# Kernel tuning notes

Measured on AMD Instinct MI355X. Metric: run time of the kernel, lower is better.

The kernel has to match this reference:

```python
import jax, jax.numpy as jnp
import numpy as np

EPS = 1e-12
B, T, D, N, FF, NH = 8, 512, 768, 6, 3072, 12
DH = D // NH  # attention head size = 64


def lin(x, w, b):
    # torch nn.Linear: y = x @ W^T + b, W: [out, in]
    return x @ w.T + b


def layer_norm(x, w, b):
    m = x.mean(-1, keepdims=True)
    v = ((x - m) ** 2).mean(-1, keepdims=True)
    return (x - m) / jnp.sqrt(v + EPS) * w + b


def conv1d(x, w, b, pad):
    # x: [B,T,D] -> conv over T with D channels -> [B,T,D]; w: [out,in,k]
    y = jax.lax.conv_general_dilated(jnp.transpose(x, (0, 2, 1)), w, (1,), [(pad, pad)],
                                     dimension_numbers=('NCH', 'OIH', 'NCH'))
    return jnp.transpose(y + b[None, :, None], (0, 2, 1))


def gelu(x):
    return jax.nn.gelu(x, approximate=False)


def setup_inputs() -> dict:
    key = jax.random.key(0)
    ks = iter(jax.random.split(key, 64))
    std = 0.02
    nrm = lambda shape: jax.random.normal(next(ks), shape, jnp.float32) * std
    inp = {}
    for i in range(N):
        inp[f'f{i}'] = jax.random.normal(next(ks), (B, T, D), jnp.float32)
    inp['Ea'] = jax.random.normal(next(ks), (B, T, D), jnp.float32)
    inp['align_w'] = nrm((N, D, D)); inp['align_b'] = jnp.zeros((N, D))
    # MultiFeatureFusion attention_fc: Linear(12, 6)
    inp['att_w'] = nrm((N, 2 * N)); inp['att_b'] = jnp.zeros((N,))
    # GatedFusion
    inp['g1_w'] = nrm((2 * D, 2 * D)); inp['g1_b'] = jnp.zeros((2 * D,))
    inp['g2_w'] = nrm((2 * D, 2 * D)); inp['g2_b'] = jnp.zeros((2 * D,))
    inp['g3_w'] = nrm((D, 2 * D)); inp['g3_b'] = jnp.zeros((D,))
    inp['g4_w'] = nrm((D, D)); inp['g4_b'] = jnp.zeros((D,))
    # MSFastformer shared LayerNorm + multi-scale convs
    inp['ln_w'] = jnp.ones((D,)); inp['ln_b'] = jnp.zeros((D,))
    inp['c1_w'] = nrm((D, D, 1)); inp['c1_b'] = jnp.zeros((D,))
    inp['c3_w'] = nrm((D, D, 3)); inp['c3_b'] = jnp.zeros((D,))
    inp['c5_w'] = nrm((D, D, 5)); inp['c5_b'] = jnp.zeros((D,))
    # FastformerLayer (shared across the three P branches)
    inp['q_w'] = nrm((D, D)); inp['q_b'] = jnp.zeros((D,))
    inp['qa_w'] = nrm((NH, D)); inp['qa_b'] = jnp.zeros((NH,))
    inp['k_w'] = nrm((D, D)); inp['k_b'] = jnp.zeros((D,))
    inp['ka_w'] = nrm((NH, D)); inp['ka_b'] = jnp.zeros((NH,))
    inp['tr_w'] = nrm((D, D)); inp['tr_b'] = jnp.zeros((D,))
    inp['ao_w'] = nrm((D, D)); inp['ao_b'] = jnp.zeros((D,))
    inp['fln_w'] = jnp.ones((D,)); inp['fln_b'] = jnp.zeros((D,))
    inp['fi_w'] = nrm((FF, D)); inp['fi_b'] = jnp.zeros((FF,))
    inp['fo_w'] = nrm((D, FF)); inp['fo_b'] = jnp.zeros((D,))
    # MSFastformer FFN + output projection
    inp['m1_w'] = nrm((FF, D)); inp['m1_b'] = jnp.zeros((FF,))
    inp['m2_w'] = nrm((D, FF)); inp['m2_b'] = jnp.zeros((D,))
    inp['out_w'] = nrm((D, D)); inp['out_b'] = jnp.zeros((D,))
    return inp


def reference(f0, f1, f2, f3, f4, f5, Ea,
              align_w, align_b, att_w, att_b,
              g1_w, g1_b, g2_w, g2_b, g3_w, g3_b, g4_w, g4_b,
              ln_w, ln_b, c1_w, c1_b, c3_w, c3_b, c5_w, c5_b,
              q_w, q_b, qa_w, qa_b, k_w, k_b, ka_w, ka_b, tr_w, tr_b, ao_w, ao_b,
              fln_w, fln_b, fi_w, fi_b, fo_w, fo_b,
              m1_w, m1_b, m2_w, m2_b, out_w, out_b):
    scale = 1.0 / (DH ** 0.5)

    def fastformer_layer(hid, ctx):
        # FastSelfAttention (note: scores contract over heads -> [B,S,Sc])
        q = lin(hid, q_w, q_b)                      # [B,S,D]
        kk = lin(ctx, k_w, k_b)                     # [B,Sc,D]
        qs = lin(q, qa_w, qa_b) * scale             # [B,S,H]
        ks = lin(kk, ka_w, ka_b) * scale            # [B,Sc,H]
        scores = jnp.einsum('bsh,bch->bsc', qs, ks)
        aw = jax.nn.softmax(scores, axis=-1)
        ctx_layer = jnp.einsum('bsc,bcd->bsd', aw, kk)
        self_out = lin(ctx_layer, tr_w, tr_b) + q
        # FastAttention residual + FFN sublayer
        att = lin(self_out, ao_w, ao_b) + hid
        att = layer_norm(att, fln_w, fln_b)
        inter = gelu(lin(att, fi_w, fi_b))
        out = lin(inter, fo_w, fo_b) + att
        return layer_norm(out, fln_w, fln_b)

    # --- FeatureAlignment: 1x1 convs (all lengths equal -> no interpolation) ---
    F6 = jnp.stack([f0, f1, f2, f3, f4, f5])                         # [N,B,T,D]
    A = jnp.einsum('nbtd,ned->nbte', F6, align_w) + align_b[:, None, None, :]
    H = jnp.transpose(A, (1, 0, 3, 2))                               # [B,N,D,T]

    # --- MultiFeatureFusion: mean_T.mean(D) and mean_D.mean(T) both equal full mean ---
    m = H.mean(axis=(2, 3))                                          # [B,N]
    mean_features = jnp.concatenate([m, m], axis=1)                  # [B,2N]
    w = jax.nn.softmax(jax.nn.relu(lin(mean_features, att_w, att_b)), axis=1)
    fused = (H * w[:, :, None, None]).sum(axis=1) + H.mean(axis=1)   # [B,D,T]
    Et = jnp.transpose(fused, (0, 2, 1))                             # [B,T,D]

    # --- GatedFusion (dropout = identity, eval mode) ---
    cc = jnp.concatenate([Et, Ea], axis=-1)
    o = jax.nn.relu(lin(cc, g1_w, g1_b))
    o = jax.nn.relu(lin(o, g2_w, g2_b))
    o = jax.nn.relu(lin(o, g3_w, g3_b))
    g = jax.nn.sigmoid(lin(o, g4_w, g4_b))
    Ef = g * Ea + (1.0 - g) * Et

    # --- MSFastformer ---
    x = layer_norm(Ef, ln_w, ln_b)
    U1 = conv1d(x, c1_w, c1_b, 0)
    U3 = conv1d(x, c3_w, c3_b, 1)
    U5 = conv1d(x, c5_w, c5_b, 2)
    P = fastformer_layer(U5, U3) + fastformer_layer(U3, U1) + fastformer_layer(U1, U5)
    Pn = layer_norm(P, ln_w, ln_b)
    I = lin(gelu(lin(Pn, m1_w, m1_b)), m2_w, m2_b)
    J = I + x
    y = lin(layer_norm(J, ln_w, ln_b), out_w, out_b)
    return y
```

## Files before the change

kernel.cpp:

```cpp
#include <hip/hip_runtime.h>
#include <math.h>


typedef unsigned short u16;
typedef __attribute__((ext_vector_type(8))) short short8;
typedef __attribute__((ext_vector_type(8))) unsigned short us8;
typedef __attribute__((ext_vector_type(4))) float floatx4;
typedef unsigned __attribute__((address_space(1))) gu32;
typedef unsigned __attribute__((address_space(3))) lu32;

#define DD 768
#define TT 512
#define BB 8
#define MM 4096
#define FFN 3072
#define MDL ((long)MM * DD)

__device__ __forceinline__ float b2f(u16 u) {
  union { unsigned u32; float f; } x; x.u32 = ((unsigned)u) << 16; return x.f;
}
__device__ __forceinline__ u16 f2b(float f) {
  union { float f; unsigned u; } x; x.f = f;
  unsigned r = x.u + 0x7FFFu + ((x.u >> 16) & 1u);
  return (u16)(r >> 16);
}

template<int BM, int BN, int OP>
__global__ __launch_bounds__(256)
void gemm_bt(const u16* __restrict__ A, const u16* __restrict__ W,
             const float* __restrict__ bias, const float* __restrict__ rowBias,
             const void* __restrict__ residv, void* __restrict__ Cv,
             int N, int K, int ldc, int rBf16, int outBf16,
             int ntaps, int pad, long wtapStride,
             long aBatch, long wBatch, long cBatch, long rBatch,
             const u16* __restrict__ zp)
{
  __shared__ __align__(16) u16 sA[2][BM * 64];
  __shared__ __align__(16) u16 sB[2][BN * 64];
  const int tid  = threadIdx.x;
  const int lane = tid & 63;
  const int wv   = tid >> 6;

  int gx = gridDim.x, gy = gridDim.y;
  int bn = blockIdx.y * gx + blockIdx.x;
  int Tt = gx * gy;
  if ((Tt & 7) == 0) bn = (bn & 7) * (Tt >> 3) + (bn >> 3);
  const int m0 = (bn / gx) * BM;
  const int n0 = (bn % gx) * BN;
  const u16* Ab  = A + (long)blockIdx.z * aBatch;
  const u16* Wb0 = W + (long)blockIdx.z * wBatch;

  constexpr int NI = (BM == 128 && BN == 128) ? 4 : (BM == 128 ? 2 : 1);
  constexpr int NJ = 4;
  int wr, wc;
  if constexpr (BM == 128 && BN == 128) { wr = (wv >> 1) * 64; wc = (wv & 1) * 64; }
  else if constexpr (BM == 128)          { wr = wv * 32;        wc = 0; }
  else                                    { wr = wv * 16;        wc = 0; }

  floatx4 acc[NI][NJ];
#pragma unroll
  for (int i = 0; i < NI; ++i)
#pragma unroll
    for (int j = 0; j < NJ; ++j) acc[i][j] = (floatx4){0.f, 0.f, 0.f, 0.f};

  const int mrow = lane & 15;
  const int ksub = (lane >> 4) * 8;

  auto STAGE = [&](int tap_, int k0_, int bsel) {
    const int dt = tap_ - pad;
    const u16* Wt = Wb0 + (long)tap_ * wtapStride;
    u16* sAb = &sA[bsel][0];
    u16* sBb = &sB[bsel][0];
#pragma unroll
    for (int it = 0; it < BM / 32; ++it) {
      int slot = it * 256 + tid;
      int row = slot >> 3;
      int col = ((slot ^ row) & 7) * 8;
      int gr = m0 + row;
      int t  = gr & (TT - 1);
      const u16* src = ((unsigned)(t + dt) < (unsigned)TT)
                     ? (Ab + (long)(gr + dt) * K + k0_ + col) : zp;
      __builtin_amdgcn_global_load_lds((const gu32*)src,
                                       (lu32*)((char*)sAb + slot * 16), 16, 0, 0);
    }
#pragma unroll
    for (int it = 0; it < BN / 32; ++it) {
      int slot = it * 256 + tid;
      int row = slot >> 3;
      int col = ((slot ^ row) & 7) * 8;
      const u16* src = Wt + (long)(n0 + row) * K + k0_ + col;
      __builtin_amdgcn_global_load_lds((const gu32*)src,
                                       (lu32*)((char*)sBb + slot * 16), 16, 0, 0);
    }
  };

  const int nk = K >> 6;
  const int nsteps = ntaps * nk;

  STAGE(0, 0, 0);
  asm volatile("s_waitcnt vmcnt(0)" ::: "memory");
  __builtin_amdgcn_s_barrier();

  int tap = 0, k0 = 0, cur = 0;
  for (int s = 0; s < nsteps; ++s) {
    int ntap = tap, nk0 = k0 + 64;
    if (nk0 >= K) { nk0 = 0; ntap = tap + 1; }
    if (s + 1 < nsteps) STAGE(ntap, nk0, cur ^ 1);
    {
      const u16* sAb = &sA[cur][0];
      const u16* sBb = &sB[cur][0];
#pragma unroll
      for (int kb = 0; kb < 64; kb += 32) {
        const int ch0 = (kb + ksub) >> 3;
        short8 af[NI], bfr[NJ];
#pragma unroll
        for (int i = 0; i < NI; ++i) {
          int ra = wr + i * 16 + mrow;
          af[i] = *(const short8*)(sAb + ra * 64 + ((ch0 ^ (ra & 7)) << 3));
        }
#pragma unroll
        for (int j = 0; j < NJ; ++j) {
          int rb = wc + j * 16 + mrow;
          bfr[j] = *(const short8*)(sBb + rb * 64 + ((ch0 ^ (rb & 7)) << 3));
        }
#pragma unroll
        for (int i = 0; i < NI; ++i)
#pragma unroll
          for (int j = 0; j < NJ; ++j)
            acc[i][j] = __builtin_amdgcn_mfma_f32_16x16x32_bf16(af[i], bfr[j], acc[i][j], 0, 0, 0);
      }
    }
    asm volatile("s_waitcnt vmcnt(0)" ::: "memory");
    __builtin_amdgcn_s_barrier();
    cur ^= 1; tap = ntap; k0 = nk0;
  }

  const int cn = lane & 15;
  const int rq = (lane >> 4) * 4;
  u16*   Ch = (u16*)Cv   + (long)blockIdx.z * cBatch;
  float* Cf = (float*)Cv + (long)blockIdx.z * cBatch;
  const long zr = (long)blockIdx.z * rBatch;
#pragma unroll
  for (int j = 0; j < NJ; ++j) {
    int gn = n0 + wc + j * 16 + cn;
    float bv = bias ? bias[gn] : 0.f;
#pragma unroll
    for (int i = 0; i < NI; ++i) {
#pragma unroll
      for (int r = 0; r < 4; ++r) {
        int gm = m0 + wr + i * 16 + rq + r;
        long idx = (long)gm * ldc + gn;
        float v = acc[i][j][r] + bv;
        if (rowBias) v += rowBias[(gm >> 9) * N + gn];
        if (residv)
          v += rBf16 ? b2f(((const u16*)residv)[idx + zr]) : ((const float*)residv)[idx + zr];
        if (OP == 1) v = fmaxf(v, 0.f);
        if (OP == 2) v = 0.5f * v * (1.f + erff(v * 0.70710678118654752440f));
        if (OP == 3) v = 1.f / (1.f + expf(-v));
        if (outBf16) Ch[idx] = f2b(v);
        else Cf[idx] = v;
      }
    }
  }
}

#define NJOBS 27
struct ConvJobs {
  const float* src[NJOBS];
  u16* dst[NJOBS];
  int n2[NJOBS];
  int rowLen2[NJOBS];
  int dstPitch2[NJOBS];
  const float* scl[NJOBS];
};
__global__ void convert_all(ConvJobs J, long total2)
{
  long g = (long)blockIdx.x * 256 + threadIdx.x;
  if (g >= total2) return;
  int j = 0; long off = g;
  while (off >= J.n2[j]) { off -= J.n2[j]; ++j; }
  long row = off / J.rowLen2[j];
  long c2  = off - row * J.rowLen2[j];
  const float4* s = (const float4*)J.src[j] + off * 2;
  float4 x = s[0], y = s[1];
  float sc = J.scl[j] ? J.scl[j][row >> 9] : 1.f;
  us8 h;
  h[0] = f2b(x.x * sc); h[1] = f2b(x.y * sc); h[2] = f2b(x.z * sc); h[3] = f2b(x.w * sc);
  h[4] = f2b(y.x * sc); h[5] = f2b(y.y * sc); h[6] = f2b(y.z * sc); h[7] = f2b(y.w * sc);
  *(us8*)(J.dst[j] + (row * (long)J.dstPitch2[j] + c2) * 8) = h;
}

__global__ void zero_kernel(u16* zp) { if (threadIdx.x < 128) zp[threadIdx.x] = 0; }

__global__ void copy16(const u16* __restrict__ s, u16* __restrict__ d)
{
  long g = (long)blockIdx.x * 256 + threadIdx.x;
  *(us8*)(d + g * 8) = *(const us8*)(s + g * 8);
}

__global__ void ln_kernel(const void* __restrict__ x, int xBf16,
                          const float* __restrict__ w, const float* __restrict__ b,
                          float* __restrict__ y32, u16* __restrict__ y16, int accum)
{
  const int row = blockIdx.x;
  const int tid = threadIdx.x;
  __shared__ float rs[256], rq[256];
  float v[3];
  long base = (long)row * DD;
  float s = 0.f, q = 0.f;
#pragma unroll
  for (int i = 0; i < 3; ++i) {
    int c = tid + i * 256;
    float t = xBf16 ? b2f(((const u16*)x)[base + c]) : ((const float*)x)[base + c];
    v[i] = t; s += t; q += t * t;
  }
  rs[tid] = s; rq[tid] = q; __syncthreads();
  for (int st = 128; st > 0; st >>= 1) {
    if (tid < st) { rs[tid] += rs[tid + st]; rq[tid] += rq[tid + st]; }
    __syncthreads();
  }
  float mean = rs[0] * (1.f / DD);
  float var  = fmaxf(rq[0] * (1.f / DD) - mean * mean, 0.f);
  float rstd = rsqrtf(var + 1e-12f);
#pragma unroll
  for (int i = 0; i < 3; ++i) {
    int c = tid + i * 256;
    float o = ((v[i] - mean) * rstd) * w[c] + b[c];
    if (y32) { if (accum) y32[base + c] += o; else y32[base + c] = o; }
    if (y16) {
      if (accum && !y32) y16[base + c] = f2b(b2f(y16[base + c]) + o);
      else y16[base + c] = f2b(o);
    }
  }
}

__global__ void ef_ln_kernel(const u16* __restrict__ g, const float* __restrict__ Ea,
                             const u16* __restrict__ EtC,
                             const float* __restrict__ w, const float* __restrict__ b,
                             u16* __restrict__ xo)
{
  const int row = blockIdx.x;
  const int tid = threadIdx.x;
  __shared__ float rs[256], rq[256];
  float v[3];
  float s = 0.f, q = 0.f;
#pragma unroll
  for (int i = 0; i < 3; ++i) {
    int c = tid + i * 256;
    float gv = b2f(g[(long)row * DD + c]);
    float et = b2f(EtC[(long)row * 1536 + c]);
    float e  = gv * Ea[(long)row * DD + c] + (1.f - gv) * et;
    v[i] = e; s += e; q += e * e;
  }
  rs[tid] = s; rq[tid] = q; __syncthreads();
  for (int st = 128; st > 0; st >>= 1) {
    if (tid < st) { rs[tid] += rs[tid + st]; rq[tid] += rq[tid + st]; }
    __syncthreads();
  }
  float mean = rs[0] * (1.f / DD);
  float var  = fmaxf(rq[0] * (1.f / DD) - mean * mean, 0.f);
  float rstd = rsqrtf(var + 1e-12f);
#pragma unroll
  for (int i = 0; i < 3; ++i) {
    int c = tid + i * 256;
    xo[(long)row * DD + c] = f2b(((v[i] - mean) * rstd) * w[c] + b[c]);
  }
}

__global__ void ln3sum_kernel(const u16* __restrict__ o,
                              const float* __restrict__ fw, const float* __restrict__ fb,
                              const float* __restrict__ lw, const float* __restrict__ lb,
                              u16* __restrict__ Pn)
{
  const int row = blockIdx.x;
  const int tid = threadIdx.x;
  __shared__ float rs[256], rq[256];
  float v[3][3], mz[3], rz[3];
  for (int z = 0; z < 3; ++z) {
    long base = (long)z * MDL + (long)row * DD;
    float s = 0.f, q = 0.f;
#pragma unroll
    for (int i = 0; i < 3; ++i) {
      int c = tid + i * 256;
      float t = b2f(o[base + c]);
      v[z][i] = t; s += t; q += t * t;
    }
    rs[tid] = s; rq[tid] = q; __syncthreads();
    for (int st = 128; st > 0; st >>= 1) {
      if (tid < st) { rs[tid] += rs[tid + st]; rq[tid] += rq[tid + st]; }
      __syncthreads();
    }
    float mean = rs[0] * (1.f / DD);
    float var  = fmaxf(rq[0] * (1.f / DD) - mean * mean, 0.f);
    mz[z] = mean; rz[z] = rsqrtf(var + 1e-12f);
    __syncthreads();
  }
  float p[3];
  float s = 0.f, q = 0.f;
#pragma unroll
  for (int i = 0; i < 3; ++i) {
    int c = tid + i * 256;
    float pv = 0.f;
#pragma unroll
    for (int z = 0; z < 3; ++z) pv += (v[z][i] - mz[z]) * rz[z];
    pv = pv * fw[c] + 3.f * fb[c];
    p[i] = pv; s += pv; q += pv * pv;
  }
  rs[tid] = s; rq[tid] = q; __syncthreads();
  for (int st = 128; st > 0; st >>= 1) {
    if (tid < st) { rs[tid] += rs[tid + st]; rq[tid] += rq[tid + st]; }
    __syncthreads();
  }
  float mean = rs[0] * (1.f / DD);
  float var  = fmaxf(rq[0] * (1.f / DD) - mean * mean, 0.f);
  float rstd = rsqrtf(var + 1e-12f);
#pragma unroll
  for (int i = 0; i < 3; ++i) {
    int c = tid + i * 256;
    Pn[(long)row * DD + c] = f2b(((p[i] - mean) * rstd) * lw[c] + lb[c]);
  }
}

__global__ void rowmean_all(const float* f0, const float* f1, const float* f2,
                            const float* f3, const float* f4, const float* f5,
                            float* __restrict__ rm)
{
  const float* fs[6] = {f0, f1, f2, f3, f4, f5};
  int n = blockIdx.y;
  int b = blockIdx.x / 3, chunk = blockIdx.x % 3;
  int d = chunk * 256 + threadIdx.x;
  const float* base = fs[n] + (long)b * TT * DD + d;
  float s = 0.f;
  for (int t = 0; t < TT; ++t) s += base[(long)t * DD];
  rm[((long)n * BB + b) * DD + d] = s * (1.f / TT);
}

__global__ void colsum_kernel(const float* __restrict__ w, float* __restrict__ cs)
{
  int n = blockIdx.x / 3, chunk = blockIdx.x % 3;
  int e = chunk * 256 + threadIdx.x;
  const float* base = w + (long)n * DD * DD + e;
  float s = 0.f;
  for (int d = 0; d < DD; ++d) s += base[(long)d * DD];
  cs[n * DD + e] = s;
}

__global__ void fusion_weights(const float* __restrict__ rm, const float* __restrict__ cs,
                               const float* __restrict__ align_b,
                               const float* __restrict__ aw, const float* __restrict__ ab,
                               float* __restrict__ wpT)
{
  __shared__ float msh[48];
  int tid = threadIdx.x;
  if (tid < 48) {
    int b = tid / 6, n = tid % 6;
    const float* r = rm + ((long)n * BB + b) * DD;
    const float* c = cs + n * DD;
    float dot = 0.f, bs = 0.f;
    for (int e = 0; e < DD; ++e) dot += r[e] * c[e];
    for (int d = 0; d < DD; ++d) bs += align_b[n * DD + d];
    msh[b * 6 + n] = (dot + bs) * (1.f / DD);
  }
  __syncthreads();
  if (tid < BB) {
    int b = tid;
    float z[6];
#pragma unroll
    for (int n = 0; n < 6; ++n) {
      float s = ab[n];
#pragma unroll
      for (int j = 0; j < 6; ++j)
        s += (aw[n * 12 + j] + aw[n * 12 + 6 + j]) * msh[b * 6 + j];
      z[n] = fmaxf(s, 0.f);
    }
    float mx = z[0];
#pragma unroll
    for (int n = 1; n < 6; ++n) mx = fmaxf(mx, z[n]);
    float se = 0.f, e[6];
#pragma unroll
    for (int n = 0; n < 6; ++n) { e[n] = expf(z[n] - mx); se += e[n]; }
#pragma unroll
    for (int n = 0; n < 6; ++n) wpT[n * 8 + b] = e[n] / se + (1.f / 6.f);
  }
}

__global__ void rowbias_kernel(const float* __restrict__ wpT, const float* __restrict__ ab,
                               float* __restrict__ rb)
{
  int b = blockIdx.x / 3;
  int d = (blockIdx.x % 3) * 256 + threadIdx.x;
  float s = 0.f;
#pragma unroll
  for (int n = 0; n < 6; ++n) s += wpT[n * 8 + b] * ab[n * DD + d];
  rb[b * DD + d] = s;
}

__global__ void repack_conv(const float* __restrict__ src, u16* __restrict__ dst, int KT)
{
  long e = (long)blockIdx.x * 256 + threadIdx.x;
  if (e >= (long)KT * DD * DD) return;
  int k = (int)(e / (DD * DD));
  int rem = (int)(e - (long)k * DD * DD);
  int o = rem / DD, i = rem % DD;
  dst[e] = f2b(src[((long)o * DD + i) * KT + k]);
}

__global__ void lin_small(const u16* __restrict__ X, const float* __restrict__ Wt,
                          const float* __restrict__ bias, float scale,
                          float* __restrict__ out)
{
  int row = blockIdx.x * 4 + (threadIdx.x >> 6);
  int lane = threadIdx.x & 63;
  float acc[12];
#pragma unroll
  for (int h = 0; h < 12; ++h) acc[h] = 0.f;
  for (int k = lane; k < DD; k += 64) {
    float xv = b2f(X[(long)row * DD + k]);
#pragma unroll
    for (int h = 0; h < 12; ++h) acc[h] += xv * Wt[h * DD + k];
  }
#pragma unroll
  for (int h = 0; h < 12; ++h)
    for (int off = 32; off > 0; off >>= 1) acc[h] += __shfl_down(acc[h], off);
  if (lane == 0) {
#pragma unroll
    for (int h = 0; h < 12; ++h)
      out[(long)row * 12 + h] = (acc[h] + bias[h]) * scale;
  }
}

__global__ void scores_softmax(const float* __restrict__ qs, const float* __restrict__ ks,
                               u16* __restrict__ aw)
{
  int bs = blockIdx.x;
  int b = bs >> 9;
  int tid = threadIdx.x;
  __shared__ float qsh[12];
  __shared__ float red[256];
  if (tid < 12) qsh[tid] = qs[(long)bs * 12 + tid];
  __syncthreads();
  float sc[2];
#pragma unroll
  for (int p = 0; p < 2; ++p) {
    int c = tid + p * 256;
    const float* kr = ks + (long)(b * 512 + c) * 12;
    float v = 0.f;
#pragma unroll
    for (int h = 0; h < 12; ++h) v += qsh[h] * kr[h];
    sc[p] = v;
  }
  red[tid] = fmaxf(sc[0], sc[1]); __syncthreads();
  for (int st = 128; st > 0; st >>= 1) {
    if (tid < st) red[tid] = fmaxf(red[tid], red[tid + st]);
    __syncthreads();
  }
  float mx = red[0]; __syncthreads();
  float e0 = expf(sc[0] - mx), e1 = expf(sc[1] - mx);
  red[tid] = e0 + e1; __syncthreads();
  for (int st = 128; st > 0; st >>= 1) {
    if (tid < st) red[tid] += red[tid + st];
    __syncthreads();
  }
  float inv = 1.f / red[0];
  aw[(long)bs * 512 + tid]       = f2b(e0 * inv);
  aw[(long)bs * 512 + tid + 256] = f2b(e1 * inv);
}

__global__ void transpose_kernel(const u16* __restrict__ in, u16* __restrict__ out)
{
  int b = blockIdx.z;
  const u16* ib = in + (long)b * TT * DD;
  u16* ob = out + (long)b * TT * DD;
  __shared__ u16 tile[32][33];
  int c0 = blockIdx.x * 32;
  int r0 = blockIdx.y * 32;
  int tx = threadIdx.x, ty = threadIdx.y;
#pragma unroll
  for (int i = 0; i < 4; ++i)
    tile[ty + 8 * i][tx] = ib[(long)(r0 + ty + 8 * i) * DD + c0 + tx];
  __syncthreads();
#pragma unroll
  for (int i = 0; i < 4; ++i)
    ob[(long)(c0 + ty + 8 * i) * TT + r0 + tx] = tile[tx][ty + 8 * i];
}

extern "C" void kernel_launch(void* const* d_in, const int* in_sizes, int n_in,
                              void* d_out, int out_size, void* d_ws, size_t ws_size,
                              hipStream_t stream)
{
  (void)in_sizes; (void)n_in; (void)out_size; (void)ws_size;
  const float* fin[6];
  for (int i = 0; i < 6; ++i) fin[i] = (const float*)d_in[i];
  const float* Ea      = (const float*)d_in[6];
  const float* align_w = (const float*)d_in[7];
  const float* align_b = (const float*)d_in[8];
  const float* att_w   = (const float*)d_in[9];
  const float* att_b   = (const float*)d_in[10];
  const float* g1_w = (const float*)d_in[11]; const float* g1_b = (const float*)d_in[12];
  const float* g2_w = (const float*)d_in[13]; const float* g2_b = (const float*)d_in[14];
  const float* g3_w = (const float*)d_in[15]; const float* g3_b = (const float*)d_in[16];
  const float* g4_w = (const float*)d_in[17]; const float* g4_b = (const float*)d_in[18];
  const float* ln_w = (const float*)d_in[19]; const float* ln_b = (const float*)d_in[20];
  const float* c1_w = (const float*)d_in[21]; const float* c1_b = (const float*)d_in[22];
  const float* c3_w = (const float*)d_in[23]; const float* c3_b = (const float*)d_in[24];
  const float* c5_w = (const float*)d_in[25]; const float* c5_b = (const float*)d_in[26];
  const float* q_w  = (const float*)d_in[27]; const float* q_b  = (const float*)d_in[28];
  const float* qa_w = (const float*)d_in[29]; const float* qa_b = (const float*)d_in[30];
  const float* k_w  = (const float*)d_in[31]; const float* k_b  = (const float*)d_in[32];
  const float* ka_w = (const float*)d_in[33]; const float* ka_b = (const float*)d_in[34];
  const float* tr_w = (const float*)d_in[35]; const float* tr_b = (const float*)d_in[36];
  const float* ao_w = (const float*)d_in[37]; const float* ao_b = (const float*)d_in[38];
  const float* fln_w = (const float*)d_in[39]; const float* fln_b = (const float*)d_in[40];
  const float* fi_w = (const float*)d_in[41]; const float* fi_b = (const float*)d_in[42];
  const float* fo_w = (const float*)d_in[43]; const float* fo_b = (const float*)d_in[44];
  const float* m1_w = (const float*)d_in[45]; const float* m1_b = (const float*)d_in[46];
  const float* m2_w = (const float*)d_in[47]; const float* m2_b = (const float*)d_in[48];
  const float* out_w = (const float*)d_in[49]; const float* out_b = (const float*)d_in[50];

  char* ws = (char*)d_ws;
  size_t off = 0;
  auto alloc = [&](size_t bytes) -> char* {
    char* p = ws + off;
    off += bytes;
    off = (off + 255) & ~(size_t)255;
    return p;
  };

  u16*   zp    = (u16*)alloc(256);
  float* rmb   = (float*)alloc(6L * BB * DD * 4);
  float* csb   = (float*)alloc(6L * DD * 4);
  float* wpT   = (float*)alloc(48 * 4);
  float* rbias = (float*)alloc((long)BB * DD * 4);
  float* qsf   = (float*)alloc(3L * MM * 12 * 4);
  float* ksf   = (float*)alloc(3L * MM * 12 * 4);

  u16* Wc = (u16*)alloc(27721728L * 2);
  u16* cW_g1   = Wc;
  u16* cW_g2   = Wc + 2359296L;
  u16* cW_fi   = Wc + 4718592L;
  u16* cW_fo   = Wc + 7077888L;
  u16* cW_m1   = Wc + 9437184L;
  u16* cW_m2   = Wc + 11796480L;
  u16* cW_g3   = Wc + 14155776L;
  u16* cW_al   = Wc + 15335424L;
  u16* cW_g4   = Wc + 18874368L;
  u16* cW_c1   = Wc + 19464192L;
  u16* cW_q    = Wc + 20054016L;
  u16* cW_k    = Wc + 20643840L;
  u16* cW_tr   = Wc + 21233664L;
  u16* cW_ao   = Wc + 21823488L;
  u16* cW_out  = Wc + 22413312L;
  u16* w3r     = Wc + 23003136L;
  u16* w5r     = Wc + 24772608L;

  char* R1 = alloc((long)MM * 4608 * 2);
  char* R3 = alloc(MDL * 8);
  char* R4 = alloc(MDL * 8);
  char* R5 = alloc(MDL * 2);
  char* R6 = alloc(MDL * 8);
  char* R8 = alloc(MDL * 6);
  char* R9 = alloc(MDL * 6);
  char* R10 = alloc((long)MM * FFN * 2);

  u16*   Ap    = (u16*)R1;
  u16*   qbuf  = (u16*)R1;
  float* Jb    = (float*)R1;
  u16*   interb3 = (u16*)R1;
  u16*   cc    = (u16*)R3;
  u16*   o1    = (u16*)R3 + 2 * MDL;
  u16*   ctxkk = (u16*)R3;
  u16*   PnB   = (u16*)R3;
  u16*   Jn    = (u16*)R3 + MDL;
  u16*   o2    = (u16*)R4;
  u16*   o3    = (u16*)R4 + 2 * MDL;
  u16*   gbuf  = (u16*)R4 + 3 * MDL;
  u16*   kkTsf = (u16*)R4;
  u16*   xb16  = (u16*)R5;
  u16*   U     = (u16*)R6;
  u16*   attp  = (u16*)R8;
  u16*   outp  = (u16*)R8;
  u16*   attb  = (u16*)R9;
  u16*   awb   = (u16*)R10;
  u16*   interb = (u16*)R10;

  auto gemm = [&](int tile, int op, const u16* A, const u16* W,
                  const float* bias, const float* rowBias,
                  const void* resid, int rB, void* Cc, int oB,
                  int Mi, int Ni, int Ki, int ldc,
                  int ntaps, int pad, long wtap,
                  int batch, long ab, long wb, long cb, long rbch) {
#define GL(BM, BN, OPV) gemm_bt<BM, BN, OPV><<<dim3(Ni / BN, Mi / BM, batch), 256, 0, stream>>>( \
      A, W, bias, rowBias, resid, Cc, Ni, Ki, ldc, rB, oB, ntaps, pad, wtap, ab, wb, cb, rbch, zp)
    if (tile == 1) {
      if (op == 0) GL(128, 64, 0); else if (op == 1) GL(128, 64, 1);
      else if (op == 2) GL(128, 64, 2); else GL(128, 64, 3);
    } else {
      if (op == 0) GL(128, 128, 0); else if (op == 1) GL(128, 128, 1);
      else if (op == 2) GL(128, 128, 2); else GL(128, 128, 3);
    }
#undef GL
  };

  zero_kernel<<<1, 128, 0, stream>>>(zp);

  rowmean_all<<<dim3(24, 6), 256, 0, stream>>>(fin[0], fin[1], fin[2], fin[3], fin[4], fin[5], rmb);
  colsum_kernel<<<18, 256, 0, stream>>>(align_w, csb);
  fusion_weights<<<1, 64, 0, stream>>>(rmb, csb, align_b, att_w, att_b, wpT);
  rowbias_kernel<<<24, 256, 0, stream>>>(wpT, align_b, rbias);

  {
    ConvJobs J;
    int idx = 0;
    long total2 = 0;
    auto add = [&](const float* s, u16* d, int n2v, int rl2, int dp2, const float* sc) {
      J.src[idx] = s; J.dst[idx] = d; J.n2[idx] = n2v;
      J.rowLen2[idx] = rl2; J.dstPitch2[idx] = dp2; J.scl[idx] = sc;
      total2 += n2v; ++idx;
    };
    for (int n = 0; n < 6; ++n)
      add(fin[n], Ap + n * DD, 393216, 96, 576, wpT + n * 8);
    add(Ea, cc + DD, 393216, 96, 192, nullptr);
    add(g1_w, cW_g1, 294912, 294912, 294912, nullptr);
    add(g2_w, cW_g2, 294912, 294912, 294912, nullptr);
    add(fi_w, cW_fi, 294912, 294912, 294912, nullptr);
    add(fo_w, cW_fo, 294912, 294912, 294912, nullptr);
    add(m1_w, cW_m1, 294912, 294912, 294912, nullptr);
    add(m2_w, cW_m2, 294912, 294912, 294912, nullptr);
    add(g3_w, cW_g3, 147456, 147456, 147456, nullptr);
    for (int n = 0; n < 6; ++n)
      add(align_w + (long)n * 589824, cW_al + n * DD, 73728, 96, 576, nullptr);
    add(g4_w, cW_g4, 73728, 73728, 73728, nullptr);
    add(c1_w, cW_c1, 73728, 73728, 73728, nullptr);
    add(q_w,  cW_q,  73728, 73728, 73728, nullptr);
    add(k_w,  cW_k,  73728, 73728, 73728, nullptr);
    add(tr_w, cW_tr, 73728, 73728, 73728, nullptr);
    add(ao_w, cW_ao, 73728, 73728, 73728, nullptr);
    add(out_w, cW_out, 73728, 73728, 73728, nullptr);
    convert_all<<<(int)((total2 + 255) / 256), 256, 0, stream>>>(J, total2);
  }
  repack_conv<<<(3 * 589824 + 255) / 256, 256, 0, stream>>>(c3_w, w3r, 3);
  repack_conv<<<(5 * 589824 + 255) / 256, 256, 0, stream>>>(c5_w, w5r, 5);

  gemm(1, 0, Ap, cW_al, nullptr, rbias, nullptr, 0, cc, 1,
       MM, DD, 4608, 1536, 1, 0, 0, 1, 0, 0, 0, 0);

  gemm(1, 1, cc, cW_g1, g1_b, nullptr, nullptr, 0, o1, 1, MM, 1536, 1536, 1536, 1, 0, 0, 1, 0, 0, 0, 0);
  gemm(1, 1, o1, cW_g2, g2_b, nullptr, nullptr, 0, o2, 1, MM, 1536, 1536, 1536, 1, 0, 0, 1, 0, 0, 0, 0);
  gemm(1, 1, o2, cW_g3, g3_b, nullptr, nullptr, 0, o3, 1, MM, DD, 1536, DD, 1, 0, 0, 1, 0, 0, 0, 0);
  gemm(1, 3, o3, cW_g4, g4_b, nullptr, nullptr, 0, gbuf, 1, MM, DD, DD, DD, 1, 0, 0, 1, 0, 0, 0, 0);
  ef_ln_kernel<<<MM, 256, 0, stream>>>(gbuf, Ea, cc, ln_w, ln_b, xb16);

  gemm(1, 0, xb16, w5r, c5_b, nullptr, nullptr, 0, U, 1, MM, DD, DD, DD, 5, 2, 589824, 1, 0, 0, 0, 0);
  gemm(1, 0, xb16, w3r, c3_b, nullptr, nullptr, 0, U + MDL, 1, MM, DD, DD, DD, 3, 1, 589824, 1, 0, 0, 0, 0);
  gemm(1, 0, xb16, cW_c1, c1_b, nullptr, nullptr, 0, U + 2 * MDL, 1, MM, DD, DD, DD, 1, 0, 0, 1, 0, 0, 0, 0);
  copy16<<<1536, 256, 0, stream>>>(U, U + 3 * MDL);

  gemm(1, 0, U,       cW_q, q_b, nullptr, nullptr, 0, qbuf,  1, MM, DD, DD, DD, 1, 0, 0, 3, MDL, 0, MDL, 0);
  gemm(1, 0, U + MDL, cW_k, k_b, nullptr, nullptr, 0, ctxkk, 1, MM, DD, DD, DD, 1, 0, 0, 3, MDL, 0, MDL, 0);
  lin_small<<<3 * MM / 4, 256, 0, stream>>>(qbuf,  qa_w, qa_b, 0.125f, qsf);
  lin_small<<<3 * MM / 4, 256, 0, stream>>>(ctxkk, ka_w, ka_b, 0.125f, ksf);
  scores_softmax<<<3 * MM, 256, 0, stream>>>(qsf, ksf, awb);
  transpose_kernel<<<dim3(24, 16, 24), dim3(32, 8), 0, stream>>>(ctxkk, kkTsf);
  gemm(1, 0, awb, kkTsf, nullptr, nullptr, nullptr, 0, ctxkk, 1, TT, DD, TT, DD,
       1, 0, 0, 24, (long)TT * TT, (long)DD * TT, (long)TT * DD, 0);
  gemm(1, 0, ctxkk, cW_tr, tr_b, nullptr, qbuf, 1, kkTsf, 1, MM, DD, DD, DD, 1, 0, 0, 3, MDL, 0, MDL, MDL);
  gemm(1, 0, kkTsf, cW_ao, ao_b, nullptr, U,    1, attp,  1, MM, DD, DD, DD, 1, 0, 0, 3, MDL, 0, MDL, MDL);
  ln_kernel<<<3 * MM, 256, 0, stream>>>(attp, 1, fln_w, fln_b, nullptr, attb, 0);
  gemm(2, 2, attb, cW_fi, fi_b, nullptr, nullptr, 0, interb3, 1,
       MM, FFN, DD, FFN, 1, 0, 0, 3, MDL, 0, (long)MM * FFN, 0);
  gemm(2, 0, interb3, cW_fo, fo_b, nullptr, attb, 1, outp, 1,
       MM, DD, FFN, DD, 1, 0, 0, 3, (long)MM * FFN, 0, MDL, MDL);
  ln3sum_kernel<<<MM, 256, 0, stream>>>(outp, fln_w, fln_b, ln_w, ln_b, PnB);

  gemm(2, 2, PnB, cW_m1, m1_b, nullptr, nullptr, 0, interb, 1, MM, FFN, DD, FFN, 1, 0, 0, 1, 0, 0, 0, 0);
  gemm(1, 0, interb, cW_m2, m2_b, nullptr, xb16, 1, Jb, 0, MM, DD, FFN, DD, 1, 0, 0, 1, 0, 0, 0, 0);
  ln_kernel<<<MM, 256, 0, stream>>>(Jb, 0, ln_w, ln_b, nullptr, Jn, 0);
  gemm(1, 0, Jn, cW_out, out_b, nullptr, nullptr, 0, d_out, 0, MM, DD, DD, DD, 1, 0, 0, 1, 0, 0, 0, 0);
}
```

Measured before the change: 1.483 ms.

## Restructure GEMM main loop with per-tap pointer increments and unrolled double-buffer pipeline

The GEMM kernel now precomputes per-thread global source pointers once per tap and advances them by 64 each k-step, instead of recomputing addresses and bounds checks inside every stage. The k-loop is unrolled by two over both LDS buffers, waits with a partial vmcnt so the next stage's loads stay in flight during compute, and raises wave priority around the MFMA block. The tap count becomes a template parameter and the zero page grows to cover the column offsets. Tile choices also change: the g1/g2 GEMMs move to 128x128 tiles and the fo GEMM to 128x64. This adds more template instantiations and an extra barrier per step. It also assumes an even number of k-steps.

```diff
diff --git a/kernel.cpp b/kernel.cpp
--- a/kernel.cpp
+++ b/kernel.cpp
@@ -25,13 +25,13 @@
   return (u16)(r >> 16);
 }
 
-template<int BM, int BN, int OP>
+template<int BM, int BN, int OP, int NTAPS>
 __global__ __launch_bounds__(256)
 void gemm_bt(const u16* __restrict__ A, const u16* __restrict__ W,
              const float* __restrict__ bias, const float* __restrict__ rowBias,
              const void* __restrict__ residv, void* __restrict__ Cv,
              int N, int K, int ldc, int rBf16, int outBf16,
-             int ntaps, int pad, long wtapStride,
+             int pad, long wtapStride,
              long aBatch, long wBatch, long cBatch, long rBatch,
              const u16* __restrict__ zp)
 {
@@ -66,73 +66,110 @@
   const int mrow = lane & 15;
   const int ksub = (lane >> 4) * 8;
 
-  auto STAGE = [&](int tap_, int k0_, int bsel) {
-    const int dt = tap_ - pad;
-    const u16* Wt = Wb0 + (long)tap_ * wtapStride;
-    u16* sAb = &sA[bsel][0];
-    u16* sBb = &sB[bsel][0];
-#pragma unroll
-    for (int it = 0; it < BM / 32; ++it) {
+  constexpr int LA = BM / 32, LB = BN / 32, LT = LA + LB;
+  const u16* aP[LA];
+  const u16* wP[LB];
+
+  auto stage = [&](u16* sAb, u16* sBb) {
+#pragma unroll
+    for (int it = 0; it < LA; ++it) {
       int slot = it * 256 + tid;
-      int row = slot >> 3;
-      int col = ((slot ^ row) & 7) * 8;
-      int gr = m0 + row;
-      int t  = gr & (TT - 1);
-      const u16* src = ((unsigned)(t + dt) < (unsigned)TT)
-                     ? (Ab + (long)(gr + dt) * K + k0_ + col) : zp;
-      __builtin_amdgcn_global_load_lds((const gu32*)src,
+      __builtin_amdgcn_global_load_lds((const gu32*)aP[it],
                                        (lu32*)((char*)sAb + slot * 16), 16, 0, 0);
-    }
-#pragma unroll
-    for (int it = 0; it < BN / 32; ++it) {
+      aP[it] += 64;
+    }
+#pragma unroll
+    for (int it = 0; it < LB; ++it) {
       int slot = it * 256 + tid;
-      int row = slot >> 3;
-      int col = ((slot ^ row) & 7) * 8;
-      const u16* src = Wt + (long)(n0 + row) * K + k0_ + col;
-      __builtin_amdgcn_global_load_lds((const gu32*)src,
+      __builtin_amdgcn_global_load_lds((const gu32*)wP[it],
                                        (lu32*)((char*)sBb + slot * 16), 16, 0, 0);
+      wP[it] += 64;
     }
   };
 
+  auto compute = [&](const u16* sAb, const u16* sBb) {
+    __builtin_amdgcn_s_setprio(1);
+#pragma unroll
+    for (int kb = 0; kb < 64; kb += 32) {
+      const int ch0 = (kb + ksub) >> 3;
+      short8 af[NI], bfr[NJ];
+#pragma unroll
+      for (int i = 0; i < NI; ++i) {
+        int ra = wr + i * 16 + mrow;
+        af[i] = *(const short8*)(sAb + ra * 64 + ((ch0 ^ (ra & 7)) << 3));
+      }
+#pragma unroll
+      for (int j = 0; j < NJ; ++j) {
+        int rb = wc + j * 16 + mrow;
+        bfr[j] = *(const short8*)(sBb + rb * 64 + ((ch0 ^ (rb & 7)) << 3));
+      }
+#pragma unroll
+      for (int i = 0; i < NI; ++i)
+#pragma unroll
+        for (int j = 0; j < NJ; ++j)
+          acc[i][j] = __builtin_amdgcn_mfma_f32_16x16x32_bf16(af[i], bfr[j], acc[i][j], 0, 0, 0);
+    }
+    __builtin_amdgcn_s_setprio(0);
+  };
+
+  auto waitp = [&]() {
+    if constexpr (LT == 6) asm volatile("s_waitcnt vmcnt(6)" ::: "memory");
+    else                   asm volatile("s_waitcnt vmcnt(8)" ::: "memory");
+  };
+
   const int nk = K >> 6;
-  const int nsteps = ntaps * nk;
-
-  STAGE(0, 0, 0);
-  asm volatile("s_waitcnt vmcnt(0)" ::: "memory");
-  __builtin_amdgcn_s_barrier();
-
-  int tap = 0, k0 = 0, cur = 0;
-  for (int s = 0; s < nsteps; ++s) {
-    int ntap = tap, nk0 = k0 + 64;
-    if (nk0 >= K) { nk0 = 0; ntap = tap + 1; }
-    if (s + 1 < nsteps) STAGE(ntap, nk0, cur ^ 1);
-    {
-      const u16* sAb = &sA[cur][0];
-      const u16* sBb = &sB[cur][0];
-#pragma unroll
-      for (int kb = 0; kb < 64; kb += 32) {
-        const int ch0 = (kb + ksub) >> 3;
-        short8 af[NI], bfr[NJ];
-#pragma unroll
-        for (int i = 0; i < NI; ++i) {
-          int ra = wr + i * 16 + mrow;
-          af[i] = *(const short8*)(sAb + ra * 64 + ((ch0 ^ (ra & 7)) << 3));
-        }
-#pragma unroll
-        for (int j = 0; j < NJ; ++j) {
-          int rb = wc + j * 16 + mrow;
-          bfr[j] = *(const short8*)(sBb + rb * 64 + ((ch0 ^ (rb & 7)) << 3));
-        }
-#pragma unroll
-        for (int i = 0; i < NI; ++i)
-#pragma unroll
-          for (int j = 0; j < NJ; ++j)
-            acc[i][j] = __builtin_amdgcn_mfma_f32_16x16x32_bf16(af[i], bfr[j], acc[i][j], 0, 0, 0);
+
+  for (int tap = 0; tap < NTAPS; ++tap) {
+    if constexpr (NTAPS == 1) {
+#pragma unroll
+      for (int it = 0; it < LA; ++it) {
+        int slot = it * 256 + tid;
+        int row = slot >> 3;
+        int col = ((slot ^ row) & 7) * 8;
+        aP[it] = Ab + (long)(m0 + row) * K + col;
       }
-    }
-    asm volatile("s_waitcnt vmcnt(0)" ::: "memory");
-    __builtin_amdgcn_s_barrier();
-    cur ^= 1; tap = ntap; k0 = nk0;
+#pragma unroll
+      for (int it = 0; it < LB; ++it) {
+        int slot = it * 256 + tid;
+        int row = slot >> 3;
+        int col = ((slot ^ row) & 7) * 8;
+        wP[it] = Wb0 + (long)(n0 + row) * K + col;
+      }
+    } else {
+      const int dt = tap - pad;
+      const u16* Wt = Wb0 + (long)tap * wtapStride;
+#pragma unroll
+      for (int it = 0; it < LA; ++it) {
+        int slot = it * 256 + tid;
+        int row = slot >> 3;
+        int col = ((slot ^ row) & 7) * 8;
+        int gr = m0 + row;
+        int t  = gr & (TT - 1);
+        aP[it] = ((unsigned)(t + dt) < (unsigned)TT)
+               ? (Ab + (long)(gr + dt) * K + col) : (zp + col);
+      }
+#pragma unroll
+      for (int it = 0; it < LB; ++it) {
+        int slot = it * 256 + tid;
+        int row = slot >> 3;
+        int col = ((slot ^ row) & 7) * 8;
+        wP[it] = Wt + (long)(n0 + row) * K + col;
+      }
+    }
+
+    stage(&sA[0][0], &sB[0][0]);
+    for (int s = 0; s < nk; s += 2) {
+      stage(&sA[1][0], &sB[1][0]);
+      waitp();
+      __builtin_amdgcn_s_barrier();
+      compute(&sA[0][0], &sB[0][0]);
+      __builtin_amdgcn_s_barrier();
+      if (s + 2 < nk) { stage(&sA[0][0], &sB[0][0]); waitp(); }
+      else asm volatile("s_waitcnt vmcnt(0)" ::: "memory");
+      __builtin_amdgcn_s_barrier();
+      compute(&sA[1][0], &sB[1][0]);
+      __builtin_amdgcn_s_barrier();
+    }
   }
 
   const int cn = lane & 15;
@@ -190,7 +227,11 @@
   *(us8*)(J.dst[j] + (row * (long)J.dstPitch2[j] + c2) * 8) = h;
 }
 
-__global__ void zero_kernel(u16* zp) { if (threadIdx.x < 128) zp[threadIdx.x] = 0; }
+__global__ void zero_kernel(u16* zp)
+{
+  int i = blockIdx.x * 256 + threadIdx.x;
+  if (i < 8192) zp[i] = 0;
+}
 
 __global__ void copy16(const u16* __restrict__ s, u16* __restrict__ d)
 {
@@ -526,7 +567,7 @@
     return p;
   };
 
-  u16*   zp    = (u16*)alloc(256);
+  u16*   zp    = (u16*)alloc(16384);
   float* rmb   = (float*)alloc(6L * BB * DD * 4);
   float* csb   = (float*)alloc(6L * DD * 4);
   float* wpT   = (float*)alloc(48 * 4);
@@ -583,25 +624,26 @@
   u16*   awb   = (u16*)R10;
   u16*   interb = (u16*)R10;
 
-  auto gemm = [&](int tile, int op, const u16* A, const u16* W,
+  auto gemm = [&](int tile, int op, int ntaps, const u16* A, const u16* W,
                   const float* bias, const float* rowBias,
                   const void* resid, int rB, void* Cc, int oB,
                   int Mi, int Ni, int Ki, int ldc,
-                  int ntaps, int pad, long wtap,
+                  int pad, long wtap,
                   int batch, long ab, long wb, long cb, long rbch) {
-#define GL(BM, BN, OPV) gemm_bt<BM, BN, OPV><<<dim3(Ni / BN, Mi / BM, batch), 256, 0, stream>>>( \
-      A, W, bias, rowBias, resid, Cc, Ni, Ki, ldc, rB, oB, ntaps, pad, wtap, ab, wb, cb, rbch, zp)
-    if (tile == 1) {
-      if (op == 0) GL(128, 64, 0); else if (op == 1) GL(128, 64, 1);
-      else if (op == 2) GL(128, 64, 2); else GL(128, 64, 3);
-    } else {
-      if (op == 0) GL(128, 128, 0); else if (op == 1) GL(128, 128, 1);
-      else if (op == 2) GL(128, 128, 2); else GL(128, 128, 3);
-    }
+#define GL(BM, BN, OPV, NT) gemm_bt<BM, BN, OPV, NT><<<dim3(Ni / BN, Mi / BM, batch), 256, 0, stream>>>( \
+      A, W, bias, rowBias, resid, Cc, Ni, Ki, ldc, rB, oB, pad, wtap, ab, wb, cb, rbch, zp)
+    if (tile == 2) {
+      if (op == 1) GL(128, 128, 1, 1);
+      else         GL(128, 128, 2, 1);
+    } else if (ntaps == 5) GL(128, 64, 0, 5);
+    else if (ntaps == 3)   GL(128, 64, 0, 3);
+    else if (op == 1)      GL(128, 64, 1, 1);
+    else if (op == 3)      GL(128, 64, 3, 1);
+    else                   GL(128, 64, 0, 1);
 #undef GL
   };
 
-  zero_kernel<<<1, 128, 0, stream>>>(zp);
+  zero_kernel<<<32, 256, 0, stream>>>(zp);
 
   rowmean_all<<<dim3(24, 6), 256, 0, stream>>>(fin[0], fin[1], fin[2], fin[3], fin[4], fin[5], rmb);
   colsum_kernel<<<18, 256, 0, stream>>>(align_w, csb);
@@ -641,39 +683,39 @@
   repack_conv<<<(3 * 589824 + 255) / 256, 256, 0, stream>>>(c3_w, w3r, 3);
   repack_conv<<<(5 * 589824 + 255) / 256, 256, 0, stream>>>(c5_w, w5r, 5);
 
-  gemm(1, 0, Ap, cW_al, nullptr, rbias, nullptr, 0, cc, 1,
-       MM, DD, 4608, 1536, 1, 0, 0, 1, 0, 0, 0, 0);
-
-  gemm(1, 1, cc, cW_g1, g1_b, nullptr, nullptr, 0, o1, 1, MM, 1536, 1536, 1536, 1, 0, 0, 1, 0, 0, 0, 0);
-  gemm(1, 1, o1, cW_g2, g2_b, nullptr, nullptr, 0, o2, 1, MM, 1536, 1536, 1536, 1, 0, 0, 1, 0, 0, 0, 0);
-  gemm(1, 1, o2, cW_g3, g3_b, nullptr, nullptr, 0, o3, 1, MM, DD, 1536, DD, 1, 0, 0, 1, 0, 0, 0, 0);
-  gemm(1, 3, o3, cW_g4, g4_b, nullptr, nullptr, 0, gbuf, 1, MM, DD, DD, DD, 1, 0, 0, 1, 0, 0, 0, 0);
+  gemm(1, 0, 1, Ap, cW_al, nullptr, rbias, nullptr, 0, cc, 1,
+       MM, DD, 4608, 1536, 0, 0, 1, 0, 0, 0, 0);
+
+  gemm(2, 1, 1, cc, cW_g1, g1_b, nullptr, nullptr, 0, o1, 1, MM, 1536, 1536, 1536, 0, 0, 1, 0, 0, 0, 0);
+  gemm(2, 1, 1, o1, cW_g2, g2_b, nullptr, nullptr, 0, o2, 1, MM, 1536, 1536, 1536, 0, 0, 1, 0, 0, 0, 0);
+  gemm(1, 1, 1, o2, cW_g3, g3_b, nullptr, nullptr, 0, o3, 1, MM, DD, 1536, DD, 0, 0, 1, 0, 0, 0, 0);
+  gemm(1, 3, 1, o3, cW_g4, g4_b, nullptr, nullptr, 0, gbuf, 1, MM, DD, DD, DD, 0, 0, 1, 0, 0, 0, 0);
   ef_ln_kernel<<<MM, 256, 0, stream>>>(gbuf, Ea, cc, ln_w, ln_b, xb16);
 
-  gemm(1, 0, xb16, w5r, c5_b, nullptr, nullptr, 0, U, 1, MM, DD, DD, DD, 5, 2, 589824, 1, 0, 0, 0, 0);
-  gemm(1, 0, xb16, w3r, c3_b, nullptr, nullptr, 0, U + MDL, 1, MM, DD, DD, DD, 3, 1, 589824, 1, 0, 0, 0, 0);
-  gemm(1, 0, xb16, cW_c1, c1_b, nullptr, nullptr, 0, U + 2 * MDL, 1, MM, DD, DD, DD, 1, 0, 0, 1, 0, 0, 0, 0);
+  gemm(1, 0, 5, xb16, w5r, c5_b, nullptr, nullptr, 0, U, 1, MM, DD, DD, DD, 2, 589824, 1, 0, 0, 0, 0);
+  gemm(1, 0, 3, xb16, w3r, c3_b, nullptr, nullptr, 0, U + MDL, 1, MM, DD, DD, DD, 1, 589824, 1, 0, 0, 0, 0);
+  gemm(1, 0, 1, xb16, cW_c1, c1_b, nullptr, nullptr, 0, U + 2 * MDL, 1, MM, DD, DD, DD, 0, 0, 1, 0, 0, 0, 0);
   copy16<<<1536, 256, 0, stream>>>(U, U + 3 * MDL);
 
-  gemm(1, 0, U,       cW_q, q_b, nullptr, nullptr, 0, qbuf,  1, MM, DD, DD, DD, 1, 0, 0, 3, MDL, 0, MDL, 0);
-  gemm(1, 0, U + MDL, cW_k, k_b, nullptr, nullptr, 0, ctxkk, 1, MM, DD, DD, DD, 1, 0, 0, 3, MDL, 0, MDL, 0);
+  gemm(1, 0, 1, U,       cW_q, q_b, nullptr, nullptr, 0, qbuf,  1, MM, DD, DD, DD, 0, 0, 3, MDL, 0, MDL, 0);
+  gemm(1, 0, 1, U + MDL, cW_k, k_b, nullptr, nullptr, 0, ctxkk, 1, MM, DD, DD, DD, 0, 0, 3, MDL, 0, MDL, 0);
   lin_small<<<3 * MM / 4, 256, 0, stream>>>(qbuf,  qa_w, qa_b, 0.125f, qsf);
   lin_small<<<3 * MM / 4, 256, 0, stream>>>(ctxkk, ka_w, ka_b, 0.125f, ksf);
   scores_softmax<<<3 * MM, 256, 0, stream>>>(qsf, ksf, awb);
   transpose_kernel<<<dim3(24, 16, 24), dim3(32, 8), 0, stream>>>(ctxkk, kkTsf);
-  gemm(1, 0, awb, kkTsf, nullptr, nullptr, nullptr, 0, ctxkk, 1, TT, DD, TT, DD,
-       1, 0, 0, 24, (long)TT * TT, (long)DD * TT, (long)TT * DD, 0);
-  gemm(1, 0, ctxkk, cW_tr, tr_b, nullptr, qbuf, 1, kkTsf, 1, MM, DD, DD, DD, 1, 0, 0, 3, MDL, 0, MDL, MDL);
-  gemm(1, 0, kkTsf, cW_ao, ao_b, nullptr, U,    1, attp,  1, MM, DD, DD, DD, 1, 0, 0, 3, MDL, 0, MDL, MDL);
+  gemm(1, 0, 1, awb, kkTsf, nullptr, nullptr, nullptr, 0, ctxkk, 1, TT, DD, TT, DD,
+       0, 0, 24, (long)TT * TT, (long)DD * TT, (long)TT * DD, 0);
+  gemm(1, 0, 1, ctxkk, cW_tr, tr_b, nullptr, qbuf, 1, kkTsf, 1, MM, DD, DD, DD, 0, 0, 3, MDL, 0, MDL, MDL);
+  gemm(1, 0, 1, kkTsf, cW_ao, ao_b, nullptr, U,    1, attp,  1, MM, DD, DD, DD, 0, 0, 3, MDL, 0, MDL, MDL);
   ln_kernel<<<3 * MM, 256, 0, stream>>>(attp, 1, fln_w, fln_b, nullptr, attb, 0);
-  gemm(2, 2, attb, cW_fi, fi_b, nullptr, nullptr, 0, interb3, 1,
-       MM, FFN, DD, FFN, 1, 0, 0, 3, MDL, 0, (long)MM * FFN, 0);
-  gemm(2, 0, interb3, cW_fo, fo_b, nullptr, attb, 1, outp, 1,
-       MM, DD, FFN, DD, 1, 0, 0, 3, (long)MM * FFN, 0, MDL, MDL);
+  gemm(2, 2, 1, attb, cW_fi, fi_b, nullptr, nullptr, 0, interb3, 1,
+       MM, FFN, DD, FFN, 0, 0, 3, MDL, 0, (long)MM * FFN, 0);
+  gemm(1, 0, 1, interb3, cW_fo, fo_b, nullptr, attb, 1, outp, 1,
+       MM, DD, FFN, DD, 0, 0, 3, (long)MM * FFN, 0, MDL, MDL);
   ln3sum_kernel<<<MM, 256, 0, stream>>>(outp, fln_w, fln_b, ln_w, ln_b, PnB);
 
-  gemm(2, 2, PnB, cW_m1, m1_b, nullptr, nullptr, 0, interb, 1, MM, FFN, DD, FFN, 1, 0, 0, 1, 0, 0, 0, 0);
-  gemm(1, 0, interb, cW_m2, m2_b, nullptr, xb16, 1, Jb, 0, MM, DD, FFN, DD, 1, 0, 0, 1, 0, 0, 0, 0);
+  gemm(2, 2, 1, PnB, cW_m1, m1_b, nullptr, nullptr, 0, interb, 1, MM, FFN, DD, FFN, 0, 0, 1, 0, 0, 0, 0);
+  gemm(1, 0, 1, interb, cW_m2, m2_b, nullptr, xb16, 1, Jb, 0, MM, DD, FFN, DD, 0, 0, 1, 0, 0, 0, 0);
   ln_kernel<<<MM, 256, 0, stream>>>(Jb, 0, ln_w, ln_b, nullptr, Jn, 0);
-  gemm(1, 0, Jn, cW_out, out_b, nullptr, nullptr, 0, d_out, 0, MM, DD, DD, DD, 1, 0, 0, 1, 0, 0, 0, 0);
-}
+  gemm(1, 0, 1, Jn, cW_out, out_b, nullptr, nullptr, 0, d_out, 0, MM, DD, DD, DD, 0, 0, 1, 0, 0, 0, 0);
+}
```

Result: faster. 1.350 ms (-8.9%).
